# Kernel optimization log

Hardware: AMD Instinct MI355X
Metric: run time of the kernel (lower is better)

Reference implementation:

```python
import jax, jax.numpy as jnp
import numpy as np

N, SEQ, E, R = 2048, 128, 512, 128


def setup_inputs() -> dict:
    key = jax.random.key(0)
    ks = jax.random.split(key, 8)
    C = jnp.sort(jax.random.randint(ks[0], (N, 2), 0, SEQ), axis=-1)  # start <= end
    L = jax.random.normal(ks[1], (N, SEQ, E), dtype=jnp.float32)
    Pos_weights = jnp.ones((N, SEQ), dtype=jnp.float32)
    Neg_weights = jnp.ones((N, SEQ), dtype=jnp.float32)
    s1 = 1.0 / np.sqrt(E)
    s2 = 1.0 / np.sqrt(R)
    W1p = jax.random.normal(ks[2], (E, R), dtype=jnp.float32) * s1
    W2p = jax.random.normal(ks[3], (R, R), dtype=jnp.float32) * s2
    W1n = jax.random.normal(ks[4], (E, R), dtype=jnp.float32) * s1
    W2n = jax.random.normal(ks[5], (R, R), dtype=jnp.float32) * s2
    Wa = jax.random.normal(ks[6], (E, R), dtype=jnp.float32) * s1
    z = jnp.zeros((R,), dtype=jnp.float32)
    return {
        'C': C, 'L': L, 'Pos_weights': Pos_weights, 'Neg_weights': Neg_weights,
        'W1p': W1p, 'b1p': z, 'W2p': W2p, 'b2p': z,
        'W1n': W1n, 'b1n': z, 'W2n': W2n, 'b2n': z,
        'Wa': Wa, 'ba': z,
    }


def _safe_cdist(x, y):
    # Euclidean distance matrix with torch.cdist semantics; zero subgradient at d=0.
    d2 = (jnp.sum(x * x, -1)[:, None] + jnp.sum(y * y, -1)[None, :]
          - 2.0 * x @ y.T)
    d2 = jnp.maximum(d2, 0.0)
    safe = jnp.where(d2 > 0, d2, 1.0)
    return jnp.where(d2 > 0, jnp.sqrt(safe), 0.0)


def _mlp2(x, W1, b1, W2, b2):
    return jnp.tanh(jnp.tanh(x @ W1 + b1) @ W2 + b2)


def reference(C, L, Pos_weights, Neg_weights,
              W1p, b1p, W2p, b2p, W1n, b1n, W2n, b2n, Wa, ba):
    t = jnp.arange(SEQ)[None, :]                  # [1, SEQ]
    start = C[:, 0:1]
    end = C[:, 1:2]
    in_region = (t >= start) & (t <= end)         # [N, SEQ]
    pos_mask = jnp.where(in_region, Pos_weights, 0.0)
    neg_mask = jnp.where(in_region, 0.0, Neg_weights)
    Pos_rep = pos_mask[..., None] * L             # [N, SEQ, E]
    Neg_rep = neg_mask[..., None] * L
    pos_t = _mlp2(Pos_rep, W1p, b1p, W2p, b2p).mean(axis=1)  # [N, R]
    neg_t = _mlp2(Neg_rep, W1n, b1n, W2n, b2n).mean(axis=1)  # [N, R]
    pos_sim = jnp.exp(-_safe_cdist(pos_t, pos_t)).sum()
    neg_sim = jnp.exp(-_safe_cdist(pos_t, neg_t)).sum()
    loss = -jnp.log(pos_sim / neg_sim)
    final_feature = jnp.tanh((Pos_rep + Neg_rep) @ Wa + ba).mean(axis=1)  # [N, R]
    return final_feature, loss
```

## Files before the change

### kernel.cpp

```cpp
#include <hip/hip_runtime.h>
#include <math.h>

#define N_   2048
#define SEQ_ 128
#define E_   512
#define R_   128
#define NR_  (N_ * R_)

typedef __attribute__((ext_vector_type(8))) short short8;
typedef __attribute__((ext_vector_type(4))) float f32x4;

typedef __attribute__((address_space(3))) void lds_t;
typedef __attribute__((address_space(1))) const void glb_t;

__device__ __forceinline__ void async16(void* l, const void* g) {
    __builtin_amdgcn_global_load_lds((glb_t*)g, (lds_t*)l, 16, 0, 0);
}

__device__ __forceinline__ ushort f2bf(float f) {
    union { float f; uint u; } v; v.f = f;
    uint r = v.u + 0x7FFFu + ((v.u >> 16) & 1u);
    return (ushort)(r >> 16);
}
__device__ __forceinline__ float fast_tanhf(float x) {
    float ax = fabsf(x);
    float t = __expf(-2.f * ax);
    float r = (1.f - t) / (1.f + t);
    return copysignf(r, x);
}

__global__ void prep_kernel(const float* __restrict__ W1p, const float* __restrict__ W1n,
                            const float* __restrict__ Wa,  const float* __restrict__ W2p,
                            const float* __restrict__ W2n, ushort* __restrict__ WT)
{
    int idx = blockIdx.x * 256 + threadIdx.x;
    if (idx < 196608) {
        int m = idx >> 16;
        int o = idx & 65535;
        int r = o >> 9, e = o & 511;
        const float* src = (m == 0) ? W1p : (m == 1) ? W1n : Wa;
        WT[idx] = f2bf(src[e * R_ + r]);
    } else if (idx < 229376) {
        int o = idx - 196608;
        int m = o >> 14;
        int p = o & 16383;
        int r = p >> 7, e = p & 127;
        const float* src = (m == 0) ? W2p : W2n;
        WT[idx] = f2bf(src[e * R_ + r]);
    }
}

__global__ __launch_bounds__(256, 3)
void mlp_mfma_kernel(const int* __restrict__ C, const float* __restrict__ L,
                     const float* __restrict__ Pw, const float* __restrict__ Nw,
                     const float* __restrict__ b1p, const float* __restrict__ b2p,
                     const float* __restrict__ b1n, const float* __restrict__ b2n,
                     const float* __restrict__ ba,  const ushort* __restrict__ WT,
                     float* __restrict__ pp, float* __restrict__ nn,
                     float* __restrict__ aa)
{
    __shared__ __align__(16) ushort lds[24576];
    __shared__ float sRed[4][128];
    __shared__ float sPm[64], sNm[64];

    const ushort* W2pT = WT + 196608;
    const ushort* W2nT = WT + 212992;

    const int bid = blockIdx.x;
    const int n = bid >> 1, half = bid & 1;
    const int tid = threadIdx.x;
    const int w = tid >> 6, l = tid & 63, q = l >> 4, c = l & 15;

    if (tid < 64) {
        int tg = half * 64 + tid;
        int c0 = C[2 * n], c1 = C[2 * n + 1];
        bool in = (tg >= c0) && (tg <= c1);
        sPm[tid] = in ? Pw[n * SEQ_ + tg] : 0.f;
        sNm[tid] = in ? 0.f : Nw[n * SEQ_ + tg];
    }

    f32x4 accP[8], accN[8], accA[8];
#pragma unroll
    for (int nt = 0; nt < 8; ++nt) { accP[nt] = 0.f; accN[nt] = 0.f; accA[nt] = 0.f; }

    const float* Lrow = L + ((size_t)(n * SEQ_ + half * 64 + w * 16 + c)) * E_ + q * 8;

    for (int ch = 0; ch < 8; ++ch) {
        const int kb = ch * 64;
#pragma unroll
        for (int j = 0; j < 12; ++j) {
            int gi = j * 4 + w;
            int s = gi >> 4, blk = gi & 15;
            int row = blk * 8 + (l >> 3);
            int kseg = (l & 7) ^ (row & 7);
            async16(&lds[(s * 128 + blk * 8) * 64], WT + s * 65536 + row * E_ + kb + kseg * 8);
        }
        const float* p0 = Lrow + kb;
        float4 xa = *(const float4*)p0;
        float4 xb = *(const float4*)(p0 + 4);
        float4 xc = *(const float4*)(p0 + 32);
        float4 xd = *(const float4*)(p0 + 36);
        short8 af0, af1;
        {
            union { short8 v; ushort u[8]; } t8;
            t8.u[0] = f2bf(xa.x); t8.u[1] = f2bf(xa.y); t8.u[2] = f2bf(xa.z); t8.u[3] = f2bf(xa.w);
            t8.u[4] = f2bf(xb.x); t8.u[5] = f2bf(xb.y); t8.u[6] = f2bf(xb.z); t8.u[7] = f2bf(xb.w);
            af0 = t8.v;
            t8.u[0] = f2bf(xc.x); t8.u[1] = f2bf(xc.y); t8.u[2] = f2bf(xc.z); t8.u[3] = f2bf(xc.w);
            t8.u[4] = f2bf(xd.x); t8.u[5] = f2bf(xd.y); t8.u[6] = f2bf(xd.z); t8.u[7] = f2bf(xd.w);
            af1 = t8.v;
        }
        __syncthreads();

#pragma unroll
        for (int k2 = 0; k2 < 2; ++k2) {
            short8 a = k2 ? af1 : af0;
            const int p = ((k2 * 4 + q) ^ (c & 7)) * 8;
#pragma unroll
            for (int nt = 0; nt < 8; ++nt) {
                int ro = (nt * 16 + c) * 64 + p;
                short8 bP = *(const short8*)&lds[ro];
                short8 bN = *(const short8*)&lds[8192 + ro];
                short8 bA = *(const short8*)&lds[16384 + ro];
                accP[nt] = __builtin_amdgcn_mfma_f32_16x16x32_bf16(a, bP, accP[nt], 0, 0, 0);
                accN[nt] = __builtin_amdgcn_mfma_f32_16x16x32_bf16(a, bN, accN[nt], 0, 0, 0);
                accA[nt] = __builtin_amdgcn_mfma_f32_16x16x32_bf16(a, bA, accA[nt], 0, 0, 0);
            }
        }
        __syncthreads();
    }

#pragma unroll
    for (int nt = 0; nt < 8; ++nt) {
        int r = nt * 16 + c;
        float bar = ba[r];
        float s = 0.f;
#pragma unroll
        for (int i = 0; i < 4; ++i) {
            int t = w * 16 + q * 4 + i;
            float m = sPm[t] + sNm[t];
            s += fast_tanhf(fmaf(m, accA[nt][i], bar));
        }
        s += __shfl_xor(s, 16);
        s += __shfl_xor(s, 32);
        if (q == 0) sRed[w][r] = s;
    }
    __syncthreads();
    if (tid < 128) {
        float v = sRed[0][tid] + sRed[1][tid] + sRed[2][tid] + sRed[3][tid];
        aa[half * NR_ + n * R_ + tid] = v * (1.f / SEQ_);
    }

    {
        ushort* sH1w = &lds[16384 + w * 2048];

#pragma unroll
        for (int ps = 0; ps < 2; ++ps) {
            const float* sM  = ps ? sNm : sPm;
            const float* b1  = ps ? b1n : b1p;
            const float* b2  = ps ? b2n : b2p;
            const ushort* W2T = ps ? W2nT : W2pT;
            float* outp = ps ? nn : pp;

            __syncthreads();

#pragma unroll
            for (int nt = 0; nt < 8; ++nt) {
                int r = nt * 16 + c;
                float b1r = b1[r];
                int rseg = r >> 3;
#pragma unroll
                for (int i = 0; i < 4; ++i) {
                    int t = q * 4 + i;
                    float m = sM[w * 16 + t];
                    float acc = ps ? accN[nt][i] : accP[nt][i];
                    float h = fast_tanhf(fmaf(m, acc, b1r));
                    int seg = rseg ^ (t & 7);
                    sH1w[t * 128 + seg * 8 + (c & 7)] = f2bf(h);
                }
            }
#pragma unroll
            for (int j = 0; j < 8; ++j) {
                int gi = j * 4 + w;
                int row = gi * 4 + (l >> 4);
                int kseg = (l & 15) ^ (row & 7);
                async16(&lds[gi * 512], W2T + row * 128 + kseg * 8);
            }
            __syncthreads();

            f32x4 acc2[8];
#pragma unroll
            for (int nt = 0; nt < 8; ++nt) acc2[nt] = 0.f;

#pragma unroll
            for (int k2 = 0; k2 < 4; ++k2) {
                const int p = ((k2 * 4 + q) ^ (c & 7)) * 8;
                short8 a = *(const short8*)&sH1w[c * 128 + p];
#pragma unroll
                for (int nt = 0; nt < 8; ++nt) {
                    short8 b = *(const short8*)&lds[(nt * 16 + c) * 128 + p];
                    acc2[nt] = __builtin_amdgcn_mfma_f32_16x16x32_bf16(a, b, acc2[nt], 0, 0, 0);
                }
            }

#pragma unroll
            for (int nt = 0; nt < 8; ++nt) {
                int r = nt * 16 + c;
                float b2r = b2[r];
                float s = 0.f;
#pragma unroll
                for (int i = 0; i < 4; ++i)
                    s += fast_tanhf(acc2[nt][i] + b2r);
                s += __shfl_xor(s, 16);
                s += __shfl_xor(s, 32);
                if (q == 0) sRed[w][r] = s;
            }
            __syncthreads();
            if (tid < 128) {
                float v = sRed[0][tid] + sRed[1][tid] + sRed[2][tid] + sRed[3][tid];
                outp[half * NR_ + n * R_ + tid] = v * (1.f / SEQ_);
            }
        }
    }
}

__global__ __launch_bounds__(256)
void ffcomb_kernel(const float* __restrict__ aa, float* __restrict__ out)
{
    int i = (blockIdx.x * 256 + threadIdx.x) * 4;
    float4 a0 = *(const float4*)(aa + i);
    float4 a1 = *(const float4*)(aa + NR_ + i);
    float4 o; o.x = a0.x + a1.x; o.y = a0.y + a1.y; o.z = a0.z + a1.z; o.w = a0.w + a1.w;
    *(float4*)(out + i) = o;
}

__global__ __launch_bounds__(256, 2)
void sim_kernel(const float* __restrict__ pp, const float* __restrict__ nn,
                float* __restrict__ simP, float* __restrict__ simN)
{
    __shared__ __align__(16) float sPi[64][133];
    __shared__ __align__(16) float sPj[32][133];
    __shared__ __align__(16) float sNj[32][133];

    const int jb = blockIdx.x;
    const int ib = blockIdx.y;
    const int tid = threadIdx.x;

#pragma unroll
    for (int it = 0; it < 8; ++it) {
        int idx = it * 256 + tid;
        int row = idx >> 5, seg = idx & 31;
        int g = (ib * 64 + row) * R_ + seg * 4;
        float4 a = *(const float4*)(pp + g);
        float4 b = *(const float4*)(pp + NR_ + g);
        a.x += b.x; a.y += b.y; a.z += b.z; a.w += b.w;
        *(float4*)&sPi[row][seg * 4] = a;
    }
#pragma unroll
    for (int it = 0; it < 4; ++it) {
        int idx = it * 256 + tid;
        int row = idx >> 5, seg = idx & 31;
        int g = (jb * 32 + row) * R_ + seg * 4;
        float4 a = *(const float4*)(pp + g);
        float4 b = *(const float4*)(pp + NR_ + g);
        a.x += b.x; a.y += b.y; a.z += b.z; a.w += b.w;
        *(float4*)&sPj[row][seg * 4] = a;
        float4 u = *(const float4*)(nn + g);
        float4 v = *(const float4*)(nn + NR_ + g);
        u.x += v.x; u.y += v.y; u.z += v.z; u.w += v.w;
        *(float4*)&sNj[row][seg * 4] = u;
    }
    __syncthreads();

    const int ty = tid >> 4, tx = tid & 15;
    float d2p[4][2] = {}, d2n[4][2] = {};

    for (int rr = 0; rr < R_; rr += 4) {
        float4 xi[4], pj[2], nj[2];
#pragma unroll
        for (int a = 0; a < 4; ++a) xi[a] = *(const float4*)&sPi[ty * 4 + a][rr];
#pragma unroll
        for (int b = 0; b < 2; ++b) {
            pj[b] = *(const float4*)&sPj[tx * 2 + b][rr];
            nj[b] = *(const float4*)&sNj[tx * 2 + b][rr];
        }
#pragma unroll
        for (int a = 0; a < 4; ++a)
#pragma unroll
            for (int b = 0; b < 2; ++b) {
                float dx;
                dx = xi[a].x - pj[b].x; d2p[a][b] = fmaf(dx, dx, d2p[a][b]);
                dx = xi[a].y - pj[b].y; d2p[a][b] = fmaf(dx, dx, d2p[a][b]);
                dx = xi[a].z - pj[b].z; d2p[a][b] = fmaf(dx, dx, d2p[a][b]);
                dx = xi[a].w - pj[b].w; d2p[a][b] = fmaf(dx, dx, d2p[a][b]);
                dx = xi[a].x - nj[b].x; d2n[a][b] = fmaf(dx, dx, d2n[a][b]);
                dx = xi[a].y - nj[b].y; d2n[a][b] = fmaf(dx, dx, d2n[a][b]);
                dx = xi[a].z - nj[b].z; d2n[a][b] = fmaf(dx, dx, d2n[a][b]);
                dx = xi[a].w - nj[b].w; d2n[a][b] = fmaf(dx, dx, d2n[a][b]);
            }
    }

    float sp = 0.f, sn = 0.f;
#pragma unroll
    for (int a = 0; a < 4; ++a)
#pragma unroll
        for (int b = 0; b < 2; ++b) {
            sp += __expf(-sqrtf(d2p[a][b]));
            sn += __expf(-sqrtf(d2n[a][b]));
        }

#pragma unroll
    for (int off = 32; off; off >>= 1) {
        sp += __shfl_down(sp, off);
        sn += __shfl_down(sn, off);
    }
    __shared__ float redP[4], redN[4];
    const int wave = tid >> 6, lane = tid & 63;
    if (lane == 0) { redP[wave] = sp; redN[wave] = sn; }
    __syncthreads();
    if (tid == 0) {
        int bidl = ib * 64 + jb;
        simP[bidl] = redP[0] + redP[1] + redP[2] + redP[3];
        simN[bidl] = redN[0] + redN[1] + redN[2] + redN[3];
    }
}

__global__ __launch_bounds__(256)
void finalize_kernel(const float* __restrict__ simP, const float* __restrict__ simN,
                     float* __restrict__ out)
{
    const int tid = threadIdx.x;
    double sp = 0.0, sn = 0.0;
    for (int i = tid; i < 2048; i += 256) { sp += (double)simP[i]; sn += (double)simN[i]; }
    __shared__ double rp[256], rn[256];
    rp[tid] = sp; rn[tid] = sn;
    __syncthreads();
    for (int s = 128; s; s >>= 1) {
        if (tid < s) { rp[tid] += rp[tid + s]; rn[tid] += rn[tid + s]; }
        __syncthreads();
    }
    if (tid == 0) out[NR_] = (float)(-log(rp[0] / rn[0]));
}

extern "C" void kernel_launch(void* const* d_in, const int* in_sizes, int n_in,
                              void* d_out, int out_size, void* d_ws, size_t ws_size,
                              hipStream_t stream)
{
    const int*   C   = (const int*)  d_in[0];
    const float* L   = (const float*)d_in[1];
    const float* Pw  = (const float*)d_in[2];
    const float* Nw  = (const float*)d_in[3];
    const float* W1p = (const float*)d_in[4];
    const float* b1p = (const float*)d_in[5];
    const float* W2p = (const float*)d_in[6];
    const float* b2p = (const float*)d_in[7];
    const float* W1n = (const float*)d_in[8];
    const float* b1n = (const float*)d_in[9];
    const float* W2n = (const float*)d_in[10];
    const float* b2n = (const float*)d_in[11];
    const float* Wa  = (const float*)d_in[12];
    const float* ba  = (const float*)d_in[13];

    float* out = (float*)d_out;
    float* pp  = (float*)d_ws;
    float* nn  = pp + 2 * NR_;
    float* aa  = nn + 2 * NR_;
    float* simP = aa + 2 * NR_;
    float* simN = simP + 2048;
    ushort* WT = (ushort*)((char*)d_ws + 6 * (size_t)NR_ * 4 + 65536);

    hipLaunchKernelGGL(prep_kernel, dim3(896), dim3(256), 0, stream,
                       W1p, W1n, Wa, W2p, W2n, WT);
    hipLaunchKernelGGL(mlp_mfma_kernel, dim3(2 * N_), dim3(256), 0, stream,
                       C, L, Pw, Nw, b1p, b2p, b1n, b2n, ba, WT, pp, nn, aa);
    hipLaunchKernelGGL(ffcomb_kernel, dim3(NR_ / 1024), dim3(256), 0, stream, aa, out);
    hipLaunchKernelGGL(sim_kernel, dim3(64, 32), dim3(256), 0, stream,
                       pp, nn, simP, simN);
    hipLaunchKernelGGL(finalize_kernel, dim3(1), dim3(256), 0, stream, simP, simN, out);
}
```

Measured before the change: 920.7 us.

## Restructure MLP kernel to 512 threads with 32x32x16 MFMA and smaller K-chunks

Reworks the main MLP kernel to use 8 waves per block, each owning a 32x32 output tile computed with 32x32x16 bf16 MFMA instead of 16x16x32. The K loop now steps 32 at a time, which halves the LDS weight buffer, and the second-layer GEMM is split across waves and K halves. It also swaps the manual bf16 rounding for the packed HIP conversion intrinsic. The aim is to cut per-wave accumulator registers and LDS footprint so more waves stay resident and latency is hidden better. The cost is more barriers per K step (16 chunks instead of 8) and extra synchronization in the second GEMM.

Result: slower. 1.134 ms (+23.1%).

```diff
diff --git a/kernel.cpp b/kernel.cpp
--- a/kernel.cpp
+++ b/kernel.cpp
@@ -1,4 +1,5 @@
 #include <hip/hip_runtime.h>
+#include <hip/hip_bf16.h>
 #include <math.h>
 
 #define N_   2048
@@ -9,6 +10,7 @@
 
 typedef __attribute__((ext_vector_type(8))) short short8;
 typedef __attribute__((ext_vector_type(4))) float f32x4;
+typedef __attribute__((ext_vector_type(16))) float f32x16;
 
 typedef __attribute__((address_space(3))) void lds_t;
 typedef __attribute__((address_space(1))) const void glb_t;
@@ -27,6 +29,14 @@
     float t = __expf(-2.f * ax);
     float r = (1.f - t) / (1.f + t);
     return copysignf(r, x);
+}
+__device__ __forceinline__ short8 cvt8(float4 a, float4 b) {
+    union { short8 v; __hip_bfloat162 h[4]; } t;
+    t.h[0] = __float22bfloat162_rn(make_float2(a.x, a.y));
+    t.h[1] = __float22bfloat162_rn(make_float2(a.z, a.w));
+    t.h[2] = __float22bfloat162_rn(make_float2(b.x, b.y));
+    t.h[3] = __float22bfloat162_rn(make_float2(b.z, b.w));
+    return t.v;
 }
 
 __global__ void prep_kernel(const float* __restrict__ W1p, const float* __restrict__ W1n,
@@ -50,7 +60,7 @@
     }
 }
 
-__global__ __launch_bounds__(256, 3)
+__global__ __launch_bounds__(512, 4)
 void mlp_mfma_kernel(const int* __restrict__ C, const float* __restrict__ L,
                      const float* __restrict__ Pw, const float* __restrict__ Nw,
                      const float* __restrict__ b1p, const float* __restrict__ b2p,
@@ -59,7 +69,7 @@
                      float* __restrict__ pp, float* __restrict__ nn,
                      float* __restrict__ aa)
 {
-    __shared__ __align__(16) ushort lds[24576];
+    __shared__ __align__(16) ushort lds[16384];
     __shared__ float sRed[4][128];
     __shared__ float sPm[64], sNm[64];
 
@@ -67,160 +77,159 @@
     const ushort* W2nT = WT + 212992;
 
     const int bid = blockIdx.x;
-    const int n = bid >> 1, half = bid & 1;
+    const int n = bid >> 1, hf = bid & 1;
     const int tid = threadIdx.x;
-    const int w = tid >> 6, l = tid & 63, q = l >> 4, c = l & 15;
+    const int w = tid >> 6, l = tid & 63;
+    const int l31 = l & 31, lh = l >> 5;
+    const int c = l & 15, q = l >> 4;
+    const int m = w >> 2, n4 = w & 3;
 
     if (tid < 64) {
-        int tg = half * 64 + tid;
+        int tg = hf * 64 + tid;
         int c0 = C[2 * n], c1 = C[2 * n + 1];
         bool in = (tg >= c0) && (tg <= c1);
         sPm[tid] = in ? Pw[n * SEQ_ + tg] : 0.f;
         sNm[tid] = in ? 0.f : Nw[n * SEQ_ + tg];
     }
 
-    f32x4 accP[8], accN[8], accA[8];
-#pragma unroll
-    for (int nt = 0; nt < 8; ++nt) { accP[nt] = 0.f; accN[nt] = 0.f; accA[nt] = 0.f; }
-
-    const float* Lrow = L + ((size_t)(n * SEQ_ + half * 64 + w * 16 + c)) * E_ + q * 8;
-
-    for (int ch = 0; ch < 8; ++ch) {
-        const int kb = ch * 64;
-#pragma unroll
-        for (int j = 0; j < 12; ++j) {
-            int gi = j * 4 + w;
-            int s = gi >> 4, blk = gi & 15;
-            int row = blk * 8 + (l >> 3);
-            int kseg = (l & 7) ^ (row & 7);
-            async16(&lds[(s * 128 + blk * 8) * 64], WT + s * 65536 + row * E_ + kb + kseg * 8);
-        }
-        const float* p0 = Lrow + kb;
-        float4 xa = *(const float4*)p0;
-        float4 xb = *(const float4*)(p0 + 4);
-        float4 xc = *(const float4*)(p0 + 32);
-        float4 xd = *(const float4*)(p0 + 36);
-        short8 af0, af1;
+    f32x16 aP = 0.f, aN = 0.f, aA = 0.f;
+
+    const float* Lrow = L + ((size_t)(n * SEQ_ + hf * 64 + m * 32 + l31)) * E_;
+
+    const int rB = n4 * 32 + l31;
+    const int RB = rB >> 1;
+    const int ub = ((rB & 1) * 4 + lh) ^ (RB & 7);
+    const int oB0 = RB * 64 + ub * 8;
+    const int oB1 = RB * 64 + (ub ^ 2) * 8;
+
+    for (int ch = 0; ch < 16; ++ch) {
+        const int kb = ch * 32;
+        const float* px = Lrow + kb + lh * 8;
+        float4 x0a = *(const float4*)px;
+        float4 x0b = *(const float4*)(px + 4);
+        float4 x1a = *(const float4*)(px + 16);
+        float4 x1b = *(const float4*)(px + 20);
+#pragma unroll
+        for (int j = 0; j < 3; ++j) {
+            int gi = j * 8 + w;
+            int s = gi >> 3, g8 = gi & 7;
+            int R = g8 * 8 + (l >> 3);
+            int u = (l & 7) ^ (R & 7);
+            int r = 2 * R + (u >> 2);
+            int tseg = u & 3;
+            async16(&lds[(s * 64 + g8 * 8) * 64], WT + s * 65536 + r * E_ + kb + tseg * 8);
+        }
+        short8 a0 = cvt8(x0a, x0b);
+        short8 a1 = cvt8(x1a, x1b);
+        __syncthreads();
         {
-            union { short8 v; ushort u[8]; } t8;
-            t8.u[0] = f2bf(xa.x); t8.u[1] = f2bf(xa.y); t8.u[2] = f2bf(xa.z); t8.u[3] = f2bf(xa.w);
-            t8.u[4] = f2bf(xb.x); t8.u[5] = f2bf(xb.y); t8.u[6] = f2bf(xb.z); t8.u[7] = f2bf(xb.w);
-            af0 = t8.v;
-            t8.u[0] = f2bf(xc.x); t8.u[1] = f2bf(xc.y); t8.u[2] = f2bf(xc.z); t8.u[3] = f2bf(xc.w);
-            t8.u[4] = f2bf(xd.x); t8.u[5] = f2bf(xd.y); t8.u[6] = f2bf(xd.z); t8.u[7] = f2bf(xd.w);
-            af1 = t8.v;
-        }
-        __syncthreads();
-
-#pragma unroll
-        for (int k2 = 0; k2 < 2; ++k2) {
-            short8 a = k2 ? af1 : af0;
-            const int p = ((k2 * 4 + q) ^ (c & 7)) * 8;
-#pragma unroll
-            for (int nt = 0; nt < 8; ++nt) {
-                int ro = (nt * 16 + c) * 64 + p;
-                short8 bP = *(const short8*)&lds[ro];
-                short8 bN = *(const short8*)&lds[8192 + ro];
-                short8 bA = *(const short8*)&lds[16384 + ro];
-                accP[nt] = __builtin_amdgcn_mfma_f32_16x16x32_bf16(a, bP, accP[nt], 0, 0, 0);
-                accN[nt] = __builtin_amdgcn_mfma_f32_16x16x32_bf16(a, bN, accN[nt], 0, 0, 0);
-                accA[nt] = __builtin_amdgcn_mfma_f32_16x16x32_bf16(a, bA, accA[nt], 0, 0, 0);
+            short8 bP0 = *(const short8*)&lds[oB0];
+            short8 bN0 = *(const short8*)&lds[4096 + oB0];
+            short8 bA0 = *(const short8*)&lds[8192 + oB0];
+            aP = __builtin_amdgcn_mfma_f32_32x32x16_bf16(a0, bP0, aP, 0, 0, 0);
+            aN = __builtin_amdgcn_mfma_f32_32x32x16_bf16(a0, bN0, aN, 0, 0, 0);
+            aA = __builtin_amdgcn_mfma_f32_32x32x16_bf16(a0, bA0, aA, 0, 0, 0);
+            short8 bP1 = *(const short8*)&lds[oB1];
+            short8 bN1 = *(const short8*)&lds[4096 + oB1];
+            short8 bA1 = *(const short8*)&lds[8192 + oB1];
+            aP = __builtin_amdgcn_mfma_f32_32x32x16_bf16(a1, bP1, aP, 0, 0, 0);
+            aN = __builtin_amdgcn_mfma_f32_32x32x16_bf16(a1, bN1, aN, 0, 0, 0);
+            aA = __builtin_amdgcn_mfma_f32_32x32x16_bf16(a1, bA1, aA, 0, 0, 0);
+        }
+        __syncthreads();
+    }
+
+    {
+        float bar_ = ba[rB];
+        float s = 0.f;
+#pragma unroll
+        for (int reg = 0; reg < 16; ++reg) {
+            int t = m * 32 + (reg & 3) + 8 * (reg >> 2) + 4 * lh;
+            float mv = sPm[t] + sNm[t];
+            s += fast_tanhf(fmaf(mv, aA[reg], bar_));
+        }
+        s += __shfl_xor(s, 32);
+        if (l < 32) sRed[m][rB] = s;
+    }
+    __syncthreads();
+    if (tid < 128)
+        aa[hf * NR_ + n * R_ + tid] = (sRed[0][tid] + sRed[1][tid]) * (1.f / SEQ_);
+
+#pragma unroll
+    for (int ps = 0; ps < 2; ++ps) {
+        const f32x16 acc1 = ps ? aN : aP;
+        const float* sM  = ps ? sNm : sPm;
+        const float* b1  = ps ? b1n : b1p;
+        const float* b2  = ps ? b2n : b2p;
+        const ushort* W2T = ps ? W2nT : W2pT;
+        float* outp = ps ? nn : pp;
+
+        {
+            float b1r = b1[rB];
+            int rlo = rB & 7, rseg = rB >> 3;
+#pragma unroll
+            for (int reg = 0; reg < 16; ++reg) {
+                int t = m * 32 + (reg & 3) + 8 * (reg >> 2) + 4 * lh;
+                float h = fast_tanhf(fmaf(sM[t], acc1[reg], b1r));
+                lds[8192 + t * 128 + ((rseg ^ (t & 7)) * 8) + rlo] = f2bf(h);
             }
         }
-        __syncthreads();
-    }
-
-#pragma unroll
-    for (int nt = 0; nt < 8; ++nt) {
-        int r = nt * 16 + c;
-        float bar = ba[r];
-        float s = 0.f;
-#pragma unroll
-        for (int i = 0; i < 4; ++i) {
-            int t = w * 16 + q * 4 + i;
-            float m = sPm[t] + sNm[t];
-            s += fast_tanhf(fmaf(m, accA[nt][i], bar));
-        }
-        s += __shfl_xor(s, 16);
-        s += __shfl_xor(s, 32);
-        if (q == 0) sRed[w][r] = s;
-    }
-    __syncthreads();
-    if (tid < 128) {
-        float v = sRed[0][tid] + sRed[1][tid] + sRed[2][tid] + sRed[3][tid];
-        aa[half * NR_ + n * R_ + tid] = v * (1.f / SEQ_);
-    }
-
-    {
-        ushort* sH1w = &lds[16384 + w * 2048];
-
-#pragma unroll
-        for (int ps = 0; ps < 2; ++ps) {
-            const float* sM  = ps ? sNm : sPm;
-            const float* b1  = ps ? b1n : b1p;
-            const float* b2  = ps ? b2n : b2p;
-            const ushort* W2T = ps ? W2nT : W2pT;
-            float* outp = ps ? nn : pp;
-
-            __syncthreads();
-
-#pragma unroll
-            for (int nt = 0; nt < 8; ++nt) {
-                int r = nt * 16 + c;
-                float b1r = b1[r];
-                int rseg = r >> 3;
-#pragma unroll
-                for (int i = 0; i < 4; ++i) {
-                    int t = q * 4 + i;
-                    float m = sM[w * 16 + t];
-                    float acc = ps ? accN[nt][i] : accP[nt][i];
-                    float h = fast_tanhf(fmaf(m, acc, b1r));
-                    int seg = rseg ^ (t & 7);
-                    sH1w[t * 128 + seg * 8 + (c & 7)] = f2bf(h);
+#pragma unroll
+        for (int j = 0; j < 2; ++j) {
+            int gi = j * 8 + w;
+            int row = gi * 8 + (l >> 3);
+            int tseg = (l & 7) ^ (row & 7);
+            async16(&lds[gi * 512], W2T + row * 128 + tseg * 8);
+        }
+        __syncthreads();
+
+        f32x4 acc2[4];
+#pragma unroll
+        for (int nt = 0; nt < 4; ++nt) acc2[nt] = 0.f;
+
+        const int arow = n4 * 16 + c;
+        const int r2base = m * 64;
+#pragma unroll
+        for (int kh = 0; kh < 2; ++kh) {
+            if (kh) {
+                __syncthreads();
+#pragma unroll
+                for (int j = 0; j < 2; ++j) {
+                    int gi = j * 8 + w;
+                    int row = gi * 8 + (l >> 3);
+                    int tseg = (l & 7) ^ (row & 7);
+                    async16(&lds[gi * 512], W2T + row * 128 + 64 + tseg * 8);
+                }
+                __syncthreads();
+            }
+#pragma unroll
+            for (int k2 = 0; k2 < 2; ++k2) {
+                int sg = kh * 8 + k2 * 4 + q;
+                short8 af = *(const short8*)&lds[8192 + arow * 128 + ((sg ^ (c & 7)) * 8)];
+#pragma unroll
+                for (int nt = 0; nt < 4; ++nt) {
+                    int r2 = r2base + nt * 16 + c;
+                    short8 bf_ = *(const short8*)&lds[r2 * 64 + (((k2 * 4 + q) ^ (c & 7)) * 8)];
+                    acc2[nt] = __builtin_amdgcn_mfma_f32_16x16x32_bf16(af, bf_, acc2[nt], 0, 0, 0);
                 }
             }
-#pragma unroll
-            for (int j = 0; j < 8; ++j) {
-                int gi = j * 4 + w;
-                int row = gi * 4 + (l >> 4);
-                int kseg = (l & 15) ^ (row & 7);
-                async16(&lds[gi * 512], W2T + row * 128 + kseg * 8);
-            }
-            __syncthreads();
-
-            f32x4 acc2[8];
-#pragma unroll
-            for (int nt = 0; nt < 8; ++nt) acc2[nt] = 0.f;
-
-#pragma unroll
-            for (int k2 = 0; k2 < 4; ++k2) {
-                const int p = ((k2 * 4 + q) ^ (c & 7)) * 8;
-                short8 a = *(const short8*)&sH1w[c * 128 + p];
-#pragma unroll
-                for (int nt = 0; nt < 8; ++nt) {
-                    short8 b = *(const short8*)&lds[(nt * 16 + c) * 128 + p];
-                    acc2[nt] = __builtin_amdgcn_mfma_f32_16x16x32_bf16(a, b, acc2[nt], 0, 0, 0);
-                }
-            }
-
-#pragma unroll
-            for (int nt = 0; nt < 8; ++nt) {
-                int r = nt * 16 + c;
-                float b2r = b2[r];
-                float s = 0.f;
-#pragma unroll
-                for (int i = 0; i < 4; ++i)
-                    s += fast_tanhf(acc2[nt][i] + b2r);
-                s += __shfl_xor(s, 16);
-                s += __shfl_xor(s, 32);
-                if (q == 0) sRed[w][r] = s;
-            }
-            __syncthreads();
-            if (tid < 128) {
-                float v = sRed[0][tid] + sRed[1][tid] + sRed[2][tid] + sRed[3][tid];
-                outp[half * NR_ + n * R_ + tid] = v * (1.f / SEQ_);
-            }
-        }
+        }
+#pragma unroll
+        for (int nt = 0; nt < 4; ++nt) {
+            int r2 = r2base + nt * 16 + c;
+            float b2r = b2[r2];
+            float s = 0.f;
+#pragma unroll
+            for (int i = 0; i < 4; ++i)
+                s += fast_tanhf(acc2[nt][i] + b2r);
+            s += __shfl_xor(s, 16);
+            s += __shfl_xor(s, 32);
+            if (q == 0) sRed[n4][r2] = s;
+        }
+        __syncthreads();
+        if (tid < 128)
+            outp[hf * NR_ + n * R_ + tid] =
+                (sRed[0][tid] + sRed[1][tid] + sRed[2][tid] + sRed[3][tid]) * (1.f / SEQ_);
     }
 }
 
@@ -371,7 +380,7 @@
 
     hipLaunchKernelGGL(prep_kernel, dim3(896), dim3(256), 0, stream,
                        W1p, W1n, Wa, W2p, W2n, WT);
-    hipLaunchKernelGGL(mlp_mfma_kernel, dim3(2 * N_), dim3(256), 0, stream,
+    hipLaunchKernelGGL(mlp_mfma_kernel, dim3(2 * N_), dim3(512), 0, stream,
                        C, L, Pw, Nw, b1p, b2p, b1n, b2n, ba, WT, pp, nn, aa);
     hipLaunchKernelGGL(ffcomb_kernel, dim3(NR_ / 1024), dim3(256), 0, stream, aa, out);
     hipLaunchKernelGGL(sim_kernel, dim3(64, 32), dim3(256), 0, stream,
```
